# Optimization experiments

Hardware: AMD Instinct MI355X
Metric: run time of the kernel (lower is better)

Reference implementation:

```python
import jax, jax.numpy as jnp
import numpy as np

B, S, D, H = 64, 197, 768, 12
HD = D // H  # 64
WIN = 14
NUM_REL = (2 * WIN - 1) ** 2 + 3  # 732


def _build_rel_index():
    ch = np.arange(WIN)
    coords = np.stack(np.meshgrid(ch, ch, indexing='ij'))  # [2, W, W]
    flat = coords.reshape(2, -1)  # [2, W*W]
    rel = flat[:, :, None] - flat[:, None, :]  # [2, W*W, W*W]
    rel = rel.transpose(1, 2, 0).astype(np.int64)
    rel[:, :, 0] += WIN - 1
    rel[:, :, 1] += WIN - 1
    rel[:, :, 0] *= 2 * WIN - 1
    idx = np.zeros((WIN * WIN + 1, WIN * WIN + 1), dtype=np.int64)
    idx[1:, 1:] = rel.sum(-1)
    idx[0, :] = NUM_REL - 3
    idx[:, 0] = NUM_REL - 2
    idx[0, 0] = NUM_REL - 1
    return idx


def setup_inputs() -> dict:
    key = jax.random.key(0)
    ks = jax.random.split(key, 7)
    s = 0.02
    return {
        'hidden_states': jax.random.normal(ks[0], (B, S, D), jnp.float32),
        'wq': jax.random.normal(ks[1], (D, D), jnp.float32) * s,
        'bq': jax.random.normal(ks[2], (D,), jnp.float32) * s,
        'wk': jax.random.normal(ks[3], (D, D), jnp.float32) * s,  # key has no bias in BEiT
        'wv': jax.random.normal(ks[4], (D, D), jnp.float32) * s,
        'bv': jax.random.normal(ks[5], (D,), jnp.float32) * s,
        'bias_table': jax.random.normal(ks[6], (NUM_REL, H), jnp.float32) * s,
        'rel_index': jnp.asarray(_build_rel_index(), jnp.int32),
    }


def reference(hidden_states, wq, bq, wk, wv, bv, bias_table, rel_index):
    def heads(x):  # [B,S,D] -> [B,H,S,HD]
        return x.reshape(B, S, H, HD).transpose(0, 2, 1, 3)

    q = heads(hidden_states @ wq.T + bq)
    k = heads(hidden_states @ wk.T)
    v = heads(hidden_states @ wv.T + bv)

    scale = 1.0 / jnp.sqrt(jnp.asarray(HD, hidden_states.dtype))
    scores = jnp.einsum('bhqd,bhkd->bhqk', q, k) * scale  # [B,H,S,S]

    # relative position bias: [S,S,H] -> [1,H,S,S]
    rel_bias = bias_table[rel_index].transpose(2, 0, 1)[None]
    scores = scores + rel_bias

    probs = jax.nn.softmax(scores, axis=-1)
    ctx = jnp.einsum('bhqk,bhkd->bhqd', probs, v)  # [B,H,S,HD]
    return ctx.transpose(0, 2, 1, 3).reshape(B, S, D)
```

## Files before the change

### kernel.cpp

```cpp
#include <hip/hip_runtime.h>


#define S_LEN 197
#define HEADS 12
#define HDIM 64
#define DMODEL 768
#define BATCH 64
#define MROWS (BATCH * S_LEN)
#define MPAD 12672
#define NCOLS (3 * DMODEL)
#define KDIM DMODEL
#define NQT 13
#define NTILE (NCOLS / 128)
#define MTILE (MPAD / 128)

typedef __attribute__((ext_vector_type(8))) short short8;
typedef __attribute__((ext_vector_type(4))) float floatx4;

#define GLD16(gp, lp)                                                                  \
  __builtin_amdgcn_global_load_lds(                                                    \
      (const __attribute__((address_space(1))) unsigned int*)(gp),                     \
      (__attribute__((address_space(3))) unsigned int*)(lp), 16, 0, 0)

__device__ __forceinline__ ushort f2bf(float f) {
  union { float f; unsigned int i; } x;
  x.f = f;
  unsigned int r = x.i + 0x7fffu + ((x.i >> 16) & 1u);
  return (ushort)(r >> 16);
}

__global__ __launch_bounds__(256) void k_prep(
    const float* __restrict__ hs, const float* __restrict__ wq,
    const float* __restrict__ wk, const float* __restrict__ wv,
    const float* __restrict__ bt, const int* __restrict__ ridx,
    ushort* __restrict__ hbf, ushort* __restrict__ wbf, float* __restrict__ biasF) {
  int gid = blockIdx.x * 256 + threadIdx.x;
  int gsz = gridDim.x * 256;
  for (int i = gid; i < MPAD * KDIM / 8; i += gsz) {
    int base = i * 8;
    int row = base / KDIM;
    ushort o[8];
    if (row < MROWS) {
      const float* s = hs + (size_t)base;
#pragma unroll
      for (int e = 0; e < 8; ++e) o[e] = f2bf(s[e]);
    } else {
#pragma unroll
      for (int e = 0; e < 8; ++e) o[e] = 0;
    }
    *(uint4*)&hbf[base] = *(const uint4*)o;
  }
  for (int i = gid; i < NCOLS * KDIM / 8; i += gsz) {
    int base = i * 8;
    int row = base / KDIM;
    int col = base - row * KDIM;
    const float* src = (row < DMODEL) ? &wq[(size_t)row * KDIM]
                       : (row < 2 * DMODEL) ? &wk[(size_t)(row - DMODEL) * KDIM]
                                            : &wv[(size_t)(row - 2 * DMODEL) * KDIM];
    ushort o[8];
#pragma unroll
    for (int e = 0; e < 8; ++e) o[e] = f2bf(src[col + e]);
    *(uint4*)&wbf[base] = *(const uint4*)o;
  }
  for (int idx = gid; idx < HEADS * NQT * NQT * 64; idx += gsz) {
    int lane = idx & 63;
    int rest = idx >> 6;
    int t = rest % NQT;
    int rest2 = rest / NQT;
    int qt = rest2 % NQT;
    int h = rest2 / NQT;
    int l16 = lane & 15, quad = lane >> 4;
    int q = qt * 16 + l16;
    floatx4 v;
#pragma unroll
    for (int r = 0; r < 4; ++r) {
      int key = t * 16 + quad * 4 + r;
      float x = -1e30f;
      if (q < S_LEN && key < S_LEN) x = bt[ridx[q * S_LEN + key] * HEADS + h];
      v[r] = x;
    }
    *(floatx4*)&biasF[(size_t)idx * 4] = v;
  }
}

__global__ __launch_bounds__(256) void k_gemm_qkv(
    const ushort* __restrict__ A, const ushort* __restrict__ W,
    const float* __restrict__ bq, const float* __restrict__ bv,
    ushort* __restrict__ Cb) {
  __shared__ __align__(16) ushort SH[128 * 128];
  ushort* As = SH;
  ushort* Bs = SH + 128 * 32;
  int tid = threadIdx.x;
  int wave = tid >> 6, lane = tid & 63;
  int quad = lane >> 4, l16 = lane & 15;

  int linear = blockIdx.y * NTILE + blockIdx.x;
  int m_t, n_t;
  if (linear < 1776) {
    int g = (linear & 7) * 222 + (linear >> 3);
    m_t = g / NTILE;
    n_t = g - m_t * NTILE;
  } else {
    m_t = linear / NTILE;
    n_t = linear - m_t * NTILE;
  }
  int m0 = m_t * 128, n0 = n_t * 128;
  int wm = (wave & 1) * 64, wn = (wave >> 1) * 64;
  int swz = (quad ^ ((l16 >> 1) & 3)) << 3;

  floatx4 acc[4][4];
  floatx4 z = {0.f, 0.f, 0.f, 0.f};
#pragma unroll
  for (int i = 0; i < 4; ++i)
#pragma unroll
    for (int j = 0; j < 4; ++j) acc[i][j] = z;

  int p0 = wave * 128 + lane;
  for (int kb = 0; kb < KDIM; kb += 32) {
    const ushort* Arow = A + (size_t)m0 * KDIM + kb;
    const ushort* Brow = W + (size_t)n0 * KDIM + kb;
#pragma unroll
    for (int s = 0; s < 2; ++s) {
      int p = p0 + s * 64;
      int r = p >> 2;
      int kc = ((p & 3) ^ ((p >> 3) & 3)) << 3;
      GLD16(&Arow[(size_t)r * KDIM + kc], &As[p * 8]);
      GLD16(&Brow[(size_t)r * KDIM + kc], &Bs[p * 8]);
    }
    __syncthreads();
    short8 af[4], bfr[4];
#pragma unroll
    for (int i = 0; i < 4; ++i) {
      af[i] = *(const short8*)(&As[(wm + i * 16 + l16) * 32 + swz]);
      bfr[i] = *(const short8*)(&Bs[(wn + i * 16 + l16) * 32 + swz]);
    }
#pragma unroll
    for (int i = 0; i < 4; ++i)
#pragma unroll
      for (int j = 0; j < 4; ++j)
        acc[i][j] = __builtin_amdgcn_mfma_f32_16x16x32_bf16(af[i], bfr[j], acc[i][j], 0, 0, 0);
    __syncthreads();
  }

#pragma unroll
  for (int j = 0; j < 4; ++j) {
    int coln = wn + j * 16 + l16;
    int col = n0 + coln;
    float bias = (col < DMODEL) ? bq[col] : ((col >= 2 * DMODEL) ? bv[col - 2 * DMODEL] : 0.f);
    float scl = (col < DMODEL) ? 0.125f : 1.0f;
#pragma unroll
    for (int i = 0; i < 4; ++i)
#pragma unroll
      for (int r = 0; r < 4; ++r) {
        int row = wm + i * 16 + quad * 4 + r;
        int ch = (coln >> 3) ^ (row & 7);
        SH[row * 128 + (ch << 3) + (coln & 7)] = f2bf((acc[i][j][r] + bias) * scl);
      }
  }
  __syncthreads();
#pragma unroll
  for (int p = 0; p < 2; ++p) {
    int row = p * 64 + wave * 16 + (lane >> 2);
    int q4 = lane & 3;
    ushort* gC = Cb + (size_t)(m0 + row) * NCOLS + n0;
#pragma unroll
    for (int c = 0; c < 4; ++c) {
      int cp = c * 4 + q4;
      int ch = cp ^ (row & 7);
      *(uint4*)&gC[cp * 8] = *(const uint4*)&SH[row * 128 + (ch << 3)];
    }
  }
}

__global__ __launch_bounds__(256) void k_attn_mfma(
    const ushort* __restrict__ Cb0, const float* __restrict__ biasF,
    float* __restrict__ out) {
  __shared__ __align__(16) ushort Vt[HDIM * 256];
  __shared__ __align__(16) ushort Ka[NQT * 2 * 512];
  int bh = blockIdx.x;
  int b = bh / HEADS, h = bh - b * HEADS;
  int tid = threadIdx.x;
  int wave = tid >> 6, lane = tid & 63;
  int quad = lane >> 4, l16 = lane & 15;
  const ushort* Cb = Cb0 + (size_t)b * S_LEN * NCOLS;
  const int qoff = h * HDIM, koff = DMODEL + h * HDIM, voff = 2 * DMODEL + h * HDIM;

  {
    uint4 z4 = {0u, 0u, 0u, 0u};
    for (int i = tid; i < HDIM * 256 / 8; i += 256) ((uint4*)Vt)[i] = z4;
  }
  __syncthreads();
  for (int idx = tid; idx < S_LEN * 32; idx += 256) {
    int key = idx >> 5, dp = (idx & 31) * 2;
    unsigned int v = *(const unsigned int*)&Cb[(size_t)key * NCOLS + voff + dp];
    int ch = key >> 3, co = key & 7;
    Vt[dp * 256 + ((ch ^ (dp & 7)) << 3) + co] = (ushort)(v & 0xffffu);
    Vt[(dp + 1) * 256 + ((ch ^ ((dp + 1) & 7)) << 3) + co] = (ushort)(v >> 16);
  }
  for (int th = wave; th < NQT * 2; th += 4) {
    int t = th >> 1, half = th & 1;
    short8 kf = *(const short8*)&Cb[(size_t)(t * 16 + l16) * NCOLS + koff + half * 32 + quad * 8];
    *(short8*)&Ka[th * 512 + lane * 8] = kf;
  }
  __syncthreads();

  for (int qt = wave; qt < NQT; qt += 4) {
    int q0 = qt * 16;
    int q = q0 + l16;
    short8 qb0 = *(const short8*)&Cb[(size_t)q * NCOLS + qoff + quad * 8];
    short8 qb1 = *(const short8*)&Cb[(size_t)q * NCOLS + qoff + 32 + quad * 8];
    const float* bF = biasF + ((size_t)((h * NQT + qt) * NQT) * 64 + lane) * 4;

    floatx4 sacc[NQT];
#pragma unroll
    for (int t = 0; t < NQT; ++t) {
      floatx4 cin = *(const floatx4*)&bF[t * 256];
      short8 ka0 = *(const short8*)&Ka[(t * 2 + 0) * 512 + lane * 8];
      short8 ka1 = *(const short8*)&Ka[(t * 2 + 1) * 512 + lane * 8];
      floatx4 s1 = __builtin_amdgcn_mfma_f32_16x16x32_bf16(ka0, qb0, cin, 0, 0, 0);
      sacc[t] = __builtin_amdgcn_mfma_f32_16x16x32_bf16(ka1, qb1, s1, 0, 0, 0);
    }

    float mx = -3e38f;
#pragma unroll
    for (int t = 0; t < NQT; ++t)
#pragma unroll
      for (int r = 0; r < 4; ++r) mx = fmaxf(mx, sacc[t][r]);
    mx = fmaxf(mx, __shfl_xor(mx, 16));
    mx = fmaxf(mx, __shfl_xor(mx, 32));
    float sum = 0.f;
    unsigned int pbf[NQT][2];
#pragma unroll
    for (int t = 0; t < NQT; ++t) {
      float e0 = __expf(sacc[t][0] - mx), e1 = __expf(sacc[t][1] - mx);
      float e2 = __expf(sacc[t][2] - mx), e3 = __expf(sacc[t][3] - mx);
      sum += (e0 + e1) + (e2 + e3);
      union { float f; unsigned int u; } a, bb, c, d;
      a.f = e0; bb.f = e1; c.f = e2; d.f = e3;
      pbf[t][0] = ((a.u + 0x8000u) >> 16) | ((bb.u + 0x8000u) & 0xffff0000u);
      pbf[t][1] = ((c.u + 0x8000u) >> 16) | ((d.u + 0x8000u) & 0xffff0000u);
    }
    sum += __shfl_xor(sum, 16);
    sum += __shfl_xor(sum, 32);
    float inv = 1.f / sum;

    floatx4 oacc[4];
    floatx4 zz = {0.f, 0.f, 0.f, 0.f};
#pragma unroll
    for (int dt = 0; dt < 4; ++dt) oacc[dt] = zz;
    int sel0 = ((quad & 1) * 2) * 16 + l16;
    int sel1 = sel0 + 16;
#pragma unroll
    for (int kk = 0; kk < 7; ++kk) {
      unsigned int u0 = 0, u1 = 0, u2 = 0, u3 = 0;
#pragma unroll
      for (int half = 0; half < 2; ++half) {
        int t = 2 * kk + half;
        if (t < NQT) {
          unsigned int v0 = __shfl((int)pbf[t][0], sel0);
          unsigned int v1 = __shfl((int)pbf[t][1], sel0);
          unsigned int v2 = __shfl((int)pbf[t][0], sel1);
          unsigned int v3 = __shfl((int)pbf[t][1], sel1);
          if ((quad >> 1) == half) { u0 = v0; u1 = v1; u2 = v2; u3 = v3; }
        }
      }
      union { uint4 u; short8 s; } pf;
      pf.u.x = u0; pf.u.y = u1; pf.u.z = u2; pf.u.w = u3;
#pragma unroll
      for (int dt = 0; dt < 4; ++dt) {
        int d = dt * 16 + l16;
        short8 vf = *(const short8*)&Vt[d * 256 + (((kk * 4 + quad) ^ (d & 7)) << 3)];
        oacc[dt] = __builtin_amdgcn_mfma_f32_16x16x32_bf16(vf, pf.s, oacc[dt], 0, 0, 0);
      }
    }

    if (q < S_LEN) {
      float* og = out + ((size_t)b * S_LEN + q) * DMODEL + h * HDIM + quad * 4;
#pragma unroll
      for (int dt = 0; dt < 4; ++dt) {
        floatx4 o = oacc[dt];
        float4 st = make_float4(o[0] * inv, o[1] * inv, o[2] * inv, o[3] * inv);
        *(float4*)&og[dt * 16] = st;
      }
    }
  }
}

extern "C" void kernel_launch(void* const* d_in, const int* in_sizes, int n_in,
                              void* d_out, int out_size, void* d_ws, size_t ws_size,
                              hipStream_t stream) {
  const float* hs = (const float*)d_in[0];
  const float* wq = (const float*)d_in[1];
  const float* bq = (const float*)d_in[2];
  const float* wk = (const float*)d_in[3];
  const float* wv = (const float*)d_in[4];
  const float* bv = (const float*)d_in[5];
  const float* bt = (const float*)d_in[6];
  const int* ridx = (const int*)d_in[7];
  float* out = (float*)d_out;

  ushort* hbf = (ushort*)d_ws;
  ushort* wbf = hbf + (size_t)MPAD * KDIM;
  ushort* Cb = wbf + (size_t)NCOLS * KDIM;
  float* biasF = (float*)(Cb + (size_t)MPAD * NCOLS);

  k_prep<<<2048, 256, 0, stream>>>(hs, wq, wk, wv, bt, ridx, hbf, wbf, biasF);
  k_gemm_qkv<<<dim3(NTILE, MTILE), 256, 0, stream>>>(hbf, wbf, bq, bv, Cb);
  k_attn_mfma<<<BATCH * HEADS, 256, 0, stream>>>(Cb, biasF, out);
}
```

Measured before the change: 237.8 us.

## Rewrite QKV GEMM as 256x256 tiles with double-buffered async LDS pipeline

The QKV projection GEMM moves from 128x128 tiles with 256 threads and a single-buffered, sync-per-k-step loop to 256x256 tiles with 512 threads (8 waves). The new loop uses 64-wide K steps, double-buffered LDS filled by global_load_lds, and staged quarter-tile issues interleaved with MFMA phases under explicit waitcnt, barriers and setprio. The grid becomes a 1D XCD-aware remap over 450 workgroups, and the A padding grows to 12800 rows to fit the larger tile. The aim is to raise arithmetic intensity and hide global load latency, at the cost of heavy register use (128 accumulator floats per thread), 128KB of LDS and fragile hand-tuned scheduling.

Measured after the change: 227.6 us. 4.3% less time.

```diff
diff --git a/kernel.cpp b/kernel.cpp
--- a/kernel.cpp
+++ b/kernel.cpp
@@ -7,12 +7,12 @@
 #define DMODEL 768
 #define BATCH 64
 #define MROWS (BATCH * S_LEN)
-#define MPAD 12672
+#define MPAD_C 12672
+#define MPAD_A 12800
 #define NCOLS (3 * DMODEL)
 #define KDIM DMODEL
 #define NQT 13
-#define NTILE (NCOLS / 128)
-#define MTILE (MPAD / 128)
+#define NWG 450
 
 typedef __attribute__((ext_vector_type(8))) short short8;
 typedef __attribute__((ext_vector_type(4))) float floatx4;
@@ -36,7 +36,7 @@
     ushort* __restrict__ hbf, ushort* __restrict__ wbf, float* __restrict__ biasF) {
   int gid = blockIdx.x * 256 + threadIdx.x;
   int gsz = gridDim.x * 256;
-  for (int i = gid; i < MPAD * KDIM / 8; i += gsz) {
+  for (int i = gid; i < MPAD_A * KDIM / 8; i += gsz) {
     int base = i * 8;
     int row = base / KDIM;
     ushort o[8];
@@ -83,91 +83,166 @@
   }
 }
 
-__global__ __launch_bounds__(256) void k_gemm_qkv(
+__global__ __launch_bounds__(512) void k_gemm_qkv(
     const ushort* __restrict__ A, const ushort* __restrict__ W,
     const float* __restrict__ bq, const float* __restrict__ bv,
     ushort* __restrict__ Cb) {
-  __shared__ __align__(16) ushort SH[128 * 128];
-  ushort* As = SH;
-  ushort* Bs = SH + 128 * 32;
+  __shared__ __align__(16) ushort SH[65536];
   int tid = threadIdx.x;
   int wave = tid >> 6, lane = tid & 63;
   int quad = lane >> 4, l16 = lane & 15;
-
-  int linear = blockIdx.y * NTILE + blockIdx.x;
-  int m_t, n_t;
-  if (linear < 1776) {
-    int g = (linear & 7) * 222 + (linear >> 3);
-    m_t = g / NTILE;
-    n_t = g - m_t * NTILE;
-  } else {
-    m_t = linear / NTILE;
-    n_t = linear - m_t * NTILE;
-  }
-  int m0 = m_t * 128, n0 = n_t * 128;
-  int wm = (wave & 1) * 64, wn = (wave >> 1) * 64;
-  int swz = (quad ^ ((l16 >> 1) & 3)) << 3;
-
-  floatx4 acc[4][4];
+  int wr = wave >> 2, wc = wave & 3;
+
+  int orig = blockIdx.x;
+  int x = orig & 7, pp = orig >> 3;
+  int wgid = (x < 2 ? x * 57 : 114 + (x - 2) * 56) + pp;
+  int m_t = wgid / 9, n_t = wgid - m_t * 9;
+  int m0 = m_t * 256, n0 = n_t * 256;
+
+  int rl = tid >> 3, ccol = tid & 7;
+  int gchunk = ccol ^ (rl & 7);
+  const ushort* srcA = A + (size_t)(m0 + rl) * KDIM + gchunk * 8;
+  const ushort* srcB = W + (size_t)(n0 + rl) * KDIM + gchunk * 8;
+  int dst0 = tid * 8;
+
+#define ISSA(u, q) GLD16(srcA + (size_t)(q) * 64 * KDIM + (u) * 64, \
+                         &SH[(((u) & 1) * 16384) + (q) * 4096 + dst0])
+#define ISSB(u, q) GLD16(srcB + (size_t)(q) * 64 * KDIM + (u) * 64, \
+                         &SH[32768 + (((u) & 1) * 16384) + (q) * 4096 + dst0])
+
+  int s7 = l16 & 7;
+  int aoff[2], boff[2];
+#pragma unroll
+  for (int ks = 0; ks < 2; ++ks) {
+    int slot = ((ks * 4 + quad) ^ s7) << 3;
+    aoff[ks] = (wr * 128 + l16) * 64 + slot;
+    boff[ks] = (wc * 64 + l16) * 64 + slot;
+  }
+
+  floatx4 acc[8][4];
   floatx4 z = {0.f, 0.f, 0.f, 0.f};
 #pragma unroll
-  for (int i = 0; i < 4; ++i)
+  for (int i = 0; i < 8; ++i)
 #pragma unroll
     for (int j = 0; j < 4; ++j) acc[i][j] = z;
 
-  int p0 = wave * 128 + lane;
-  for (int kb = 0; kb < KDIM; kb += 32) {
-    const ushort* Arow = A + (size_t)m0 * KDIM + kb;
-    const ushort* Brow = W + (size_t)n0 * KDIM + kb;
-#pragma unroll
-    for (int s = 0; s < 2; ++s) {
-      int p = p0 + s * 64;
-      int r = p >> 2;
-      int kc = ((p & 3) ^ ((p >> 3) & 3)) << 3;
-      GLD16(&Arow[(size_t)r * KDIM + kc], &As[p * 8]);
-      GLD16(&Brow[(size_t)r * KDIM + kc], &Bs[p * 8]);
-    }
+  ISSA(0, 0); ISSA(0, 1); ISSA(0, 2); ISSA(0, 3);
+  ISSB(0, 0); ISSB(0, 1); ISSB(0, 2); ISSB(0, 3);
+  ISSA(1, 0); ISSA(1, 2);
+  ISSB(1, 0); ISSB(1, 1); ISSB(1, 2); ISSB(1, 3);
+  asm volatile("s_waitcnt vmcnt(6)" ::: "memory");
+  __builtin_amdgcn_s_barrier();
+  asm volatile("" ::: "memory");
+
+#pragma unroll 2
+  for (int t = 0; t < 12; ++t) {
+    const ushort* Ab = &SH[(t & 1) * 16384];
+    const ushort* Bb = &SH[32768 + (t & 1) * 16384];
+    short8 a0[2][4], a1[2][4], b0[2][2], b1[2][2];
+#pragma unroll
+    for (int ks = 0; ks < 2; ++ks) {
+#pragma unroll
+      for (int i = 0; i < 4; ++i) a0[ks][i] = *(const short8*)&Ab[aoff[ks] + i * 1024];
+#pragma unroll
+      for (int j = 0; j < 2; ++j) b0[ks][j] = *(const short8*)&Bb[boff[ks] + j * 1024];
+    }
+    if (t <= 10) { ISSA(t + 1, 1); ISSA(t + 1, 3); }
+    asm volatile("s_waitcnt lgkmcnt(8)" ::: "memory");
+    __builtin_amdgcn_s_barrier();
+    asm volatile("s_waitcnt lgkmcnt(0)" ::: "memory");
+    __builtin_amdgcn_s_setprio(1);
+#pragma unroll
+    for (int i = 0; i < 4; ++i)
+#pragma unroll
+      for (int j = 0; j < 2; ++j) {
+        acc[i][j] = __builtin_amdgcn_mfma_f32_16x16x32_bf16(a0[0][i], b0[0][j], acc[i][j], 0, 0, 0);
+        acc[i][j] = __builtin_amdgcn_mfma_f32_16x16x32_bf16(a0[1][i], b0[1][j], acc[i][j], 0, 0, 0);
+      }
+    __builtin_amdgcn_s_setprio(0);
+    __builtin_amdgcn_s_barrier();
+#pragma unroll
+    for (int ks = 0; ks < 2; ++ks)
+#pragma unroll
+      for (int j = 0; j < 2; ++j) b1[ks][j] = *(const short8*)&Bb[boff[ks] + (2 + j) * 1024];
+    if (t <= 9) { ISSA(t + 2, 0); ISSA(t + 2, 2); }
+    __builtin_amdgcn_s_barrier();
+    asm volatile("s_waitcnt lgkmcnt(0)" ::: "memory");
+    __builtin_amdgcn_s_setprio(1);
+#pragma unroll
+    for (int i = 0; i < 4; ++i)
+#pragma unroll
+      for (int j = 0; j < 2; ++j) {
+        acc[i][2 + j] = __builtin_amdgcn_mfma_f32_16x16x32_bf16(a0[0][i], b1[0][j], acc[i][2 + j], 0, 0, 0);
+        acc[i][2 + j] = __builtin_amdgcn_mfma_f32_16x16x32_bf16(a0[1][i], b1[1][j], acc[i][2 + j], 0, 0, 0);
+      }
+    __builtin_amdgcn_s_setprio(0);
+    __builtin_amdgcn_s_barrier();
+#pragma unroll
+    for (int ks = 0; ks < 2; ++ks)
+#pragma unroll
+      for (int i = 0; i < 4; ++i) a1[ks][i] = *(const short8*)&Ab[aoff[ks] + (4 + i) * 1024];
+    if (t <= 9) { ISSB(t + 2, 0); ISSB(t + 2, 1); }
+    __builtin_amdgcn_s_barrier();
+    asm volatile("s_waitcnt lgkmcnt(0)" ::: "memory");
+    __builtin_amdgcn_s_setprio(1);
+#pragma unroll
+    for (int i = 0; i < 4; ++i)
+#pragma unroll
+      for (int j = 0; j < 2; ++j) {
+        acc[4 + i][2 + j] = __builtin_amdgcn_mfma_f32_16x16x32_bf16(a1[0][i], b1[0][j], acc[4 + i][2 + j], 0, 0, 0);
+        acc[4 + i][2 + j] = __builtin_amdgcn_mfma_f32_16x16x32_bf16(a1[1][i], b1[1][j], acc[4 + i][2 + j], 0, 0, 0);
+      }
+    __builtin_amdgcn_s_setprio(0);
+    __builtin_amdgcn_s_barrier();
+    if (t <= 9) { ISSB(t + 2, 2); ISSB(t + 2, 3); }
+    __builtin_amdgcn_s_barrier();
+    __builtin_amdgcn_s_setprio(1);
+#pragma unroll
+    for (int i = 0; i < 4; ++i)
+#pragma unroll
+      for (int j = 0; j < 2; ++j) {
+        acc[4 + i][j] = __builtin_amdgcn_mfma_f32_16x16x32_bf16(a1[0][i], b0[0][j], acc[4 + i][j], 0, 0, 0);
+        acc[4 + i][j] = __builtin_amdgcn_mfma_f32_16x16x32_bf16(a1[1][i], b0[1][j], acc[4 + i][j], 0, 0, 0);
+      }
+    __builtin_amdgcn_s_setprio(0);
+    if (t <= 9) asm volatile("s_waitcnt vmcnt(6)" ::: "memory");
+    else        asm volatile("s_waitcnt vmcnt(0)" ::: "memory");
+    __builtin_amdgcn_s_barrier();
+    asm volatile("" ::: "memory");
+  }
+#undef ISSA
+#undef ISSB
+
+#pragma unroll
+  for (int P = 0; P < 2; ++P) {
     __syncthreads();
-    short8 af[4], bfr[4];
-#pragma unroll
-    for (int i = 0; i < 4; ++i) {
-      af[i] = *(const short8*)(&As[(wm + i * 16 + l16) * 32 + swz]);
-      bfr[i] = *(const short8*)(&Bs[(wn + i * 16 + l16) * 32 + swz]);
-    }
-#pragma unroll
-    for (int i = 0; i < 4; ++i)
-#pragma unroll
-      for (int j = 0; j < 4; ++j)
-        acc[i][j] = __builtin_amdgcn_mfma_f32_16x16x32_bf16(af[i], bfr[j], acc[i][j], 0, 0, 0);
+    if (wr == P) {
+#pragma unroll
+      for (int j = 0; j < 4; ++j) {
+        int cn = wc * 64 + j * 16 + l16;
+        int col = n0 + cn;
+        float bias = (col < DMODEL) ? bq[col] : ((col >= 2 * DMODEL) ? bv[col - 2 * DMODEL] : 0.f);
+        float scl = (col < DMODEL) ? 0.125f : 1.0f;
+#pragma unroll
+        for (int i = 0; i < 8; ++i)
+#pragma unroll
+          for (int r = 0; r < 4; ++r) {
+            int lr = i * 16 + quad * 4 + r;
+            int ch = (cn >> 3) ^ (lr & 7);
+            SH[lr * 256 + (ch << 3) + (cn & 7)] = f2bf((acc[i][j][r] + bias) * scl);
+          }
+      }
+    }
     __syncthreads();
-  }
-
-#pragma unroll
-  for (int j = 0; j < 4; ++j) {
-    int coln = wn + j * 16 + l16;
-    int col = n0 + coln;
-    float bias = (col < DMODEL) ? bq[col] : ((col >= 2 * DMODEL) ? bv[col - 2 * DMODEL] : 0.f);
-    float scl = (col < DMODEL) ? 0.125f : 1.0f;
-#pragma unroll
-    for (int i = 0; i < 4; ++i)
-#pragma unroll
-      for (int r = 0; r < 4; ++r) {
-        int row = wm + i * 16 + quad * 4 + r;
-        int ch = (coln >> 3) ^ (row & 7);
-        SH[row * 128 + (ch << 3) + (coln & 7)] = f2bf((acc[i][j][r] + bias) * scl);
-      }
-  }
-  __syncthreads();
-#pragma unroll
-  for (int p = 0; p < 2; ++p) {
-    int row = p * 64 + wave * 16 + (lane >> 2);
-    int q4 = lane & 3;
-    ushort* gC = Cb + (size_t)(m0 + row) * NCOLS + n0;
-#pragma unroll
-    for (int c = 0; c < 4; ++c) {
-      int cp = c * 4 + q4;
-      int ch = cp ^ (row & 7);
-      *(uint4*)&gC[cp * 8] = *(const uint4*)&SH[row * 128 + (ch << 3)];
+#pragma unroll
+    for (int k = 0; k < 8; ++k) {
+      int c0 = k * 512 + tid;
+      int lr = c0 >> 5, ch = c0 & 31;
+      int grow = m0 + P * 128 + lr;
+      if (grow < MPAD_C) {
+        *(uint4*)&Cb[(size_t)grow * NCOLS + n0 + ch * 8] =
+            *(const uint4*)&SH[lr * 256 + ((ch ^ (lr & 7)) << 3)];
+      }
     }
   }
 }
@@ -300,11 +375,11 @@
   float* out = (float*)d_out;
 
   ushort* hbf = (ushort*)d_ws;
-  ushort* wbf = hbf + (size_t)MPAD * KDIM;
+  ushort* wbf = hbf + (size_t)MPAD_A * KDIM;
   ushort* Cb = wbf + (size_t)NCOLS * KDIM;
-  float* biasF = (float*)(Cb + (size_t)MPAD * NCOLS);
+  float* biasF = (float*)(Cb + (size_t)MPAD_C * NCOLS);
 
   k_prep<<<2048, 256, 0, stream>>>(hs, wq, wk, wv, bt, ridx, hbf, wbf, biasF);
-  k_gemm_qkv<<<dim3(NTILE, MTILE), 256, 0, stream>>>(hbf, wbf, bq, bv, Cb);
+  k_gemm_qkv<<<NWG, 512, 0, stream>>>(hbf, wbf, bq, bv, Cb);
   k_attn_mfma<<<BATCH * HEADS, 256, 0, stream>>>(Cb, biasF, out);
 }
```
